# Performance work log

Measured on AMD Instinct MI355X. Metric: run time of the kernel, lower is better.

The kernel has to match this reference:

```python
import jax, jax.numpy as jnp
import numpy as np

B, S, D = 2, 2048, 1024
H, HD = 16, 64          # num_heads, head_dim = D // H
C = 8                   # subspace_dim of the equivariant relative-position basis
EPS = 1e-6              # flax LayerNorm default epsilon


def setup_inputs() -> dict:
    key = jax.random.key(0)
    ks = jax.random.split(key, 12)
    sd = 0.02
    return {
        "x": jax.random.normal(ks[0], (B, S, D), jnp.float32),
        "Q_basis": jax.random.normal(ks[1], (S, S, C), jnp.float32),
        "Wq": jax.random.normal(ks[2], (D, H, HD), jnp.float32) * sd,
        "bq": jnp.zeros((H, HD), jnp.float32),
        "Wk": jax.random.normal(ks[3], (D, H, HD), jnp.float32) * sd,
        "bk": jnp.zeros((H, HD), jnp.float32),
        "Wv": jax.random.normal(ks[4], (D, H, HD), jnp.float32) * sd,
        "bv": jnp.zeros((H, HD), jnp.float32),
        "q_ln_scale": jnp.ones((HD,), jnp.float32),
        "k_ln_scale": jnp.ones((HD,), jnp.float32),
        "relative_attn": jax.random.normal(ks[5], (C, H), jnp.float32) * sd,
        "Wo": jax.random.normal(ks[6], (H, HD, D), jnp.float32) * sd,
        "bo": jnp.zeros((D,), jnp.float32),
    }


def _layernorm(x, scale):
    # LayerNorm over last axis, use_bias=False
    mu = jnp.mean(x, axis=-1, keepdims=True)
    var = jnp.mean(jnp.square(x - mu), axis=-1, keepdims=True)
    return (x - mu) * jax.lax.rsqrt(var + EPS) * scale


def reference(x, Q_basis, Wq, bq, Wk, bk, Wv, bv,
              q_ln_scale, k_ln_scale, relative_attn, Wo, bo):
    # QKV projections: [B,S,D] x [D,H,HD] -> [B,S,H,HD]
    q = jnp.einsum('bsd,dhk->bshk', x, Wq) + bq
    k = jnp.einsum('bsd,dhk->bshk', x, Wk) + bk
    v = jnp.einsum('bsd,dhk->bshk', x, Wv) + bv
    # QK layernorm over head_dim
    q = _layernorm(q, q_ln_scale)
    k = _layernorm(k, k_ln_scale)
    # Learned relative-position bias: [C,H] x [S,S,C] -> [H,S,S]
    bias = jnp.einsum('ch,qkc->hqk', relative_attn, Q_basis)
    # Scaled dot-product attention with bias (matches nn.dot_product_attention)
    scores = jnp.einsum('bqhd,bkhd->bhqk', q, k) / jnp.sqrt(jnp.float32(HD))
    attn = jax.nn.softmax(scores + bias, axis=-1)
    ctx = jnp.einsum('bhqk,bkhd->bqhd', attn, v)
    # Output projection over (heads, head_dim) -> D
    return jnp.einsum('bqhd,hdo->bqo', ctx, Wo) + bo
```

## Files before the change

kernel.cpp:

```cpp
#include <hip/hip_runtime.h>

typedef float f32x4 __attribute__((ext_vector_type(4)));
typedef __bf16 bf16x8 __attribute__((ext_vector_type(8)));
typedef unsigned short u16x8 __attribute__((ext_vector_type(8)));
typedef unsigned short u16x4 __attribute__((ext_vector_type(4)));

#define AS1 __attribute__((address_space(1)))
#define AS3 __attribute__((address_space(3)))

static __device__ __forceinline__ void gll16(const void* g, void* l) {
  __builtin_amdgcn_global_load_lds((const AS1 void*)g, (AS3 void*)l, 16, 0, 0);
}

static __device__ __forceinline__ float bf2f(unsigned short u) {
  unsigned int x = ((unsigned int)u) << 16;
  float f; __builtin_memcpy(&f, &x, 4); return f;
}
static __device__ __forceinline__ unsigned short f2bf(float f) {
  unsigned int x; __builtin_memcpy(&x, &f, 4);
  unsigned int r = (x + 0x7fffu + ((x >> 16) & 1u)) >> 16;
  return (unsigned short)r;
}

#define LOG2E 1.4426950408889634f
#define QSCALE (0.125f * LOG2E)

__global__ __launch_bounds__(256) void k_cvt_x(const float* __restrict__ x,
                                               unsigned short* __restrict__ xb) {
  int i = (blockIdx.x * 256 + threadIdx.x) * 4;
  float4 v = *(const float4*)(x + i);
  u16x4 o; o.x = f2bf(v.x); o.y = f2bf(v.y); o.z = f2bf(v.z); o.w = f2bf(v.w);
  *(u16x4*)(xb + i) = o;
}

__global__ __launch_bounds__(256) void k_transpose(const float* __restrict__ w0,
                                                   const float* __restrict__ w1,
                                                   const float* __restrict__ w2,
                                                   const float* __restrict__ w3,
                                                   unsigned short* __restrict__ dqkv,
                                                   unsigned short* __restrict__ dwo) {
  __shared__ float tile[32][33];
  int z = blockIdx.z;
  const float* src = (z == 0) ? w0 : (z == 1) ? w1 : (z == 2) ? w2 : w3;
  unsigned short* dst = (z < 3) ? (dqkv + (size_t)z * 1024 * 1024) : dwo;
  int tx = threadIdx.x, ty = threadIdx.y;
  int x0 = blockIdx.x * 32, y0 = blockIdx.y * 32;
#pragma unroll
  for (int i = 0; i < 4; ++i)
    tile[ty + 8 * i][tx] = src[(size_t)(y0 + ty + 8 * i) * 1024 + x0 + tx];
  __syncthreads();
#pragma unroll
  for (int i = 0; i < 4; ++i)
    dst[(size_t)(x0 + ty + 8 * i) * 1024 + y0 + tx] = f2bf(tile[tx][ty + 8 * i]);
}

__global__ __launch_bounds__(256) void k_bias(const float* __restrict__ Qb,
                                              const float* __restrict__ R,
                                              unsigned short* __restrict__ bias) {
  __shared__ float Rs[8][16];
  int t = threadIdx.x;
  if (t < 128) Rs[t >> 4][t & 15] = R[t] * LOG2E;
  __syncthreads();
  int q = blockIdx.x;
  int k = t * 8;
  const float* src = Qb + ((size_t)q * 2048 + k) * 8;
  float a[8][8];
#pragma unroll
  for (int kk = 0; kk < 8; ++kk) {
    float4 lo = *(const float4*)(src + kk * 8);
    float4 hi = *(const float4*)(src + kk * 8 + 4);
    a[kk][0] = lo.x; a[kk][1] = lo.y; a[kk][2] = lo.z; a[kk][3] = lo.w;
    a[kk][4] = hi.x; a[kk][5] = hi.y; a[kk][6] = hi.z; a[kk][7] = hi.w;
  }
#pragma unroll
  for (int h = 0; h < 16; ++h) {
    u16x8 o;
#pragma unroll
    for (int kk = 0; kk < 8; ++kk) {
      float s = 0.f;
#pragma unroll
      for (int c = 0; c < 8; ++c) s += a[kk][c] * Rs[c][h];
      o[kk] = f2bf(s);
    }
    *(u16x8*)(bias + ((size_t)h * 2048 + q) * 2048 + k) = o;
  }
}

__global__ __launch_bounds__(256) void k_qkv(const unsigned short* __restrict__ xb,
                                             const unsigned short* __restrict__ wt,
                                             const float* __restrict__ bq,
                                             const float* __restrict__ bk,
                                             const float* __restrict__ bv,
                                             const float* __restrict__ qls,
                                             const float* __restrict__ kls,
                                             unsigned short* __restrict__ qo,
                                             unsigned short* __restrict__ kqo,
                                             unsigned short* __restrict__ vo) {
  __shared__ __align__(16) unsigned short As[8192];
  __shared__ __align__(16) unsigned short Bs[8192];
  const int tid = threadIdx.x;
  const int w = tid >> 6, lane = tid & 63, quad = lane >> 4, lx = lane & 15;
  const int m0 = blockIdx.y * 128, n0 = blockIdx.x * 128;
  const int wrow = w >> 1, wcol = w & 1;

  f32x4 acc[4][4];
#pragma unroll
  for (int i = 0; i < 4; ++i)
#pragma unroll
    for (int j = 0; j < 4; ++j) acc[i][j] = (f32x4){0.f, 0.f, 0.f, 0.f};

  const unsigned short* ga = xb + (size_t)(m0 + 32 * w + (lane >> 2)) * 1024 + (lane & 3) * 8;
  const unsigned short* gb = wt + (size_t)(n0 + 32 * w + (lane >> 2)) * 1024 + (lane & 3) * 8;

  gll16(ga, As + w * 1024);
  gll16(ga + 16 * 1024, As + w * 1024 + 512);
  gll16(gb, Bs + w * 1024);
  gll16(gb + 16 * 1024, Bs + w * 1024 + 512);
  __syncthreads();

  for (int kt = 0; kt < 32; ++kt) {
    const int cur = kt & 1;
    if (kt < 31) {
      const int kofs = (kt + 1) * 32;
      unsigned short* lan = As + (cur ^ 1) * 4096 + w * 1024;
      unsigned short* lbn = Bs + (cur ^ 1) * 4096 + w * 1024;
      gll16(ga + kofs, lan);
      gll16(ga + kofs + 16 * 1024, lan + 512);
      gll16(gb + kofs, lbn);
      gll16(gb + kofs + 16 * 1024, lbn + 512);
    }
    const unsigned short* ac = As + cur * 4096;
    const unsigned short* bc = Bs + cur * 4096;
    bf16x8 af[4], bfr[4];
#pragma unroll
    for (int i = 0; i < 4; ++i)
      af[i] = *(const bf16x8*)&ac[(64 * wrow + 16 * i + lx) * 32 + quad * 8];
#pragma unroll
    for (int j = 0; j < 4; ++j)
      bfr[j] = *(const bf16x8*)&bc[(64 * wcol + 16 * j + lx) * 32 + quad * 8];
    __builtin_amdgcn_s_setprio(1);
#pragma unroll
    for (int i = 0; i < 4; ++i)
#pragma unroll
      for (int j = 0; j < 4; ++j)
        acc[i][j] = __builtin_amdgcn_mfma_f32_16x16x32_bf16(af[i], bfr[j], acc[i][j], 0, 0, 0);
    __builtin_amdgcn_s_setprio(0);
    __syncthreads();
  }

  const int colbase = n0 + 64 * wcol;
  const int region = colbase >> 10;
  const int h = (colbase & 1023) >> 6;
  const float* pbp = (region == 0) ? bq : (region == 1) ? bk : bv;
  float pb[4];
#pragma unroll
  for (int j = 0; j < 4; ++j) pb[j] = pbp[h * 64 + j * 16 + lx];

  if (region == 2) {
#pragma unroll
    for (int i = 0; i < 4; ++i) {
#pragma unroll
      for (int rr = 0; rr < 4; ++rr) {
        int m = m0 + 64 * wrow + 16 * i + quad * 4 + rr;
        int b = m >> 11, s = m & 2047;
        unsigned short* dst = vo + ((size_t)b * 16 + h) * 64 * 2048 + s;
#pragma unroll
        for (int j = 0; j < 4; ++j)
          dst[(size_t)(j * 16 + lx) * 2048] = f2bf(acc[i][j][rr] + pb[j]);
      }
    }
  } else {
    const float fac = region ? 1.0f : QSCALE;
    float scl[4];
    const float* lsp = region ? kls : qls;
#pragma unroll
    for (int j = 0; j < 4; ++j) scl[j] = lsp[j * 16 + lx] * fac;
    unsigned short* base = region ? kqo : qo;
#pragma unroll
    for (int i = 0; i < 4; ++i) {
#pragma unroll
      for (int rr = 0; rr < 4; ++rr) {
        int m = m0 + 64 * wrow + 16 * i + quad * 4 + rr;
        int b = m >> 11, s = m & 2047;
        float v0 = acc[i][0][rr] + pb[0];
        float v1 = acc[i][1][rr] + pb[1];
        float v2 = acc[i][2][rr] + pb[2];
        float v3 = acc[i][3][rr] + pb[3];
        float s1 = v0 + v1 + v2 + v3;
        float s2 = v0 * v0 + v1 * v1 + v2 * v2 + v3 * v3;
#pragma unroll
        for (int d = 1; d < 16; d <<= 1) {
          s1 += __shfl_xor(s1, d, 64);
          s2 += __shfl_xor(s2, d, 64);
        }
        float mu = s1 * 0.015625f;
        float var = s2 * 0.015625f - mu * mu;
        float ri = __builtin_amdgcn_rsqf(var + 1e-6f);
        unsigned short* dst = base + (((size_t)b * 16 + h) * 2048 + s) * 64;
        dst[0 * 16 + lx] = f2bf((v0 - mu) * ri * scl[0]);
        dst[1 * 16 + lx] = f2bf((v1 - mu) * ri * scl[1]);
        dst[2 * 16 + lx] = f2bf((v2 - mu) * ri * scl[2]);
        dst[3 * 16 + lx] = f2bf((v3 - mu) * ri * scl[3]);
      }
    }
  }
}

__global__ __launch_bounds__(256) void k_attn(const unsigned short* __restrict__ qp,
                                              const unsigned short* __restrict__ kp,
                                              const unsigned short* __restrict__ vp,
                                              const unsigned short* __restrict__ bp,
                                              unsigned short* __restrict__ ctx) {
  __shared__ __align__(16) unsigned short QPs[4096];
  __shared__ __align__(16) unsigned short Ks[8192];
  __shared__ __align__(16) unsigned short Vs[8192];
  const int tid = threadIdx.x;
  const int w = tid >> 6, lane = tid & 63, quad = lane >> 4, lx = lane & 15;
  const int lx7 = lane & 7;
  const int qt = blockIdx.x, h = blockIdx.y, b = blockIdx.z;
  const int q0 = qt * 64;
  const size_t bh = (size_t)b * 16 + h;

  const unsigned short* qg = qp + (bh * 2048 + q0) * 64;
  gll16(qg + w * 512 + lane * 8, QPs + w * 512);
  gll16(qg + 2048 + w * 512 + lane * 8, QPs + 2048 + w * 512);

  const unsigned short* kg = kp + bh * 2048 * 64;
  const unsigned short* vg = vp + bh * 64 * 2048;
  const unsigned short* bg = bp + ((size_t)h * 2048 + q0 + 16 * w + quad * 4) * 2048 + lx;

  const int rA = 16 * w + (lane >> 3);
  const int cA = (lane & 7) ^ (rA & 7);
  const unsigned short* kgA = kg + (size_t)rA * 64 + cA * 8;
  const unsigned short* kgB = kg + (size_t)(rA + 8) * 64 + cA * 8;
  const unsigned short* vgA = vg + (size_t)rA * 2048 + cA * 8;
  const unsigned short* vgB = vg + (size_t)(rA + 8) * 2048 + cA * 8;

  gll16(kgA, Ks + w * 1024);
  gll16(kgB, Ks + w * 1024 + 512);
  gll16(vgA, Vs + w * 1024);
  gll16(vgB, Vs + w * 1024 + 512);
  unsigned short bu[4][4], bun[4][4];
#pragma unroll
  for (int rr = 0; rr < 4; ++rr)
#pragma unroll
    for (int j = 0; j < 4; ++j) bu[rr][j] = bg[(size_t)rr * 2048 + j * 16];

  __syncthreads();

  bf16x8 qf[2];
#pragma unroll
  for (int hh = 0; hh < 2; ++hh)
    qf[hh] = *(const bf16x8*)&QPs[(16 * w + lx) * 64 + hh * 32 + quad * 8];

  float l_run[4] = {0.f, 0.f, 0.f, 0.f};
  f32x4 acco[4];
#pragma unroll
  for (int j = 0; j < 4; ++j) acco[j] = (f32x4){0.f, 0.f, 0.f, 0.f};

  for (int kt = 0; kt < 32; ++kt) {
    const int cur = kt & 1;
    const unsigned short* kc = Ks + cur * 4096;
    const unsigned short* vc = Vs + cur * 4096;
    if (kt < 31) {
      const size_t k1 = (size_t)(kt + 1) * 64;
      unsigned short* kn = Ks + (cur ^ 1) * 4096 + w * 1024;
      unsigned short* vn = Vs + (cur ^ 1) * 4096 + w * 1024;
      gll16(kgA + k1 * 64, kn);
      gll16(kgB + k1 * 64, kn + 512);
      gll16(vgA + k1, vn);
      gll16(vgB + k1, vn + 512);
#pragma unroll
      for (int rr = 0; rr < 4; ++rr)
#pragma unroll
        for (int j = 0; j < 4; ++j) bun[rr][j] = bg[(size_t)rr * 2048 + k1 + j * 16];
    }

    f32x4 accs[4];
#pragma unroll
    for (int j = 0; j < 4; ++j)
#pragma unroll
      for (int rr = 0; rr < 4; ++rr) accs[j][rr] = bf2f(bu[rr][j]);
    __builtin_amdgcn_s_setprio(1);
#pragma unroll
    for (int j = 0; j < 4; ++j) {
#pragma unroll
      for (int hh = 0; hh < 2; ++hh) {
        bf16x8 kf = *(const bf16x8*)&kc[(j * 16 + lx) * 64 + ((hh * 4 + quad) ^ lx7) * 8];
        accs[j] = __builtin_amdgcn_mfma_f32_16x16x32_bf16(qf[hh], kf, accs[j], 0, 0, 0);
      }
    }
    __builtin_amdgcn_s_setprio(0);

#pragma unroll
    for (int rr = 0; rr < 4; ++rr) {
      float p0 = __builtin_amdgcn_exp2f(accs[0][rr]);
      float p1 = __builtin_amdgcn_exp2f(accs[1][rr]);
      float p2 = __builtin_amdgcn_exp2f(accs[2][rr]);
      float p3 = __builtin_amdgcn_exp2f(accs[3][rr]);
      l_run[rr] += (p0 + p1) + (p2 + p3);
      const int q = quad * 4 + rr;
      const int swz = q & 7;
      const int ch = lx >> 3;
      unsigned short* pw = QPs + w * 1024 + q * 64 + (lx & 7);
      pw[((ch ^ swz) << 3)]       = f2bf(p0);
      pw[(((ch + 2) ^ swz) << 3)] = f2bf(p1);
      pw[(((ch + 4) ^ swz) << 3)] = f2bf(p2);
      pw[(((ch + 6) ^ swz) << 3)] = f2bf(p3);
    }
    __asm__ volatile("s_waitcnt lgkmcnt(0)" ::: "memory");
    bf16x8 pf[2];
#pragma unroll
    for (int kh = 0; kh < 2; ++kh)
      pf[kh] = *(const bf16x8*)&QPs[w * 1024 + lx * 64 + (((kh * 4 + quad) ^ (lx & 7)) << 3)];
    __builtin_amdgcn_s_setprio(1);
#pragma unroll
    for (int j = 0; j < 4; ++j) {
#pragma unroll
      for (int kh = 0; kh < 2; ++kh) {
        bf16x8 vf = *(const bf16x8*)&vc[(j * 16 + lx) * 64 + ((kh * 4 + quad) ^ lx7) * 8];
        acco[j] = __builtin_amdgcn_mfma_f32_16x16x32_bf16(pf[kh], vf, acco[j], 0, 0, 0);
      }
    }
    __builtin_amdgcn_s_setprio(0);
    __syncthreads();
#pragma unroll
    for (int rr = 0; rr < 4; ++rr)
#pragma unroll
      for (int j = 0; j < 4; ++j) bu[rr][j] = bun[rr][j];
  }

#pragma unroll
  for (int rr = 0; rr < 4; ++rr) {
    float l = l_run[rr];
#pragma unroll
    for (int d = 1; d < 16; d <<= 1) l += __shfl_xor(l, d, 64);
    float rl = __builtin_amdgcn_rcpf(l);
    int s = q0 + 16 * w + quad * 4 + rr;
    unsigned short* dst = ctx + (((size_t)b * 2048 + s) * 16 + h) * 64;
#pragma unroll
    for (int j = 0; j < 4; ++j) dst[j * 16 + lx] = f2bf(acco[j][rr] * rl);
  }
}

__global__ __launch_bounds__(256) void k_out(const unsigned short* __restrict__ cx,
                                             const unsigned short* __restrict__ wt,
                                             const float* __restrict__ bo,
                                             float* __restrict__ out) {
  __shared__ __align__(16) unsigned short As[8192];
  __shared__ __align__(16) unsigned short Bs[8192];
  const int tid = threadIdx.x;
  const int w = tid >> 6, lane = tid & 63, quad = lane >> 4, lx = lane & 15;
  const int m0 = blockIdx.y * 128, n0 = blockIdx.x * 128;
  const int wrow = w >> 1, wcol = w & 1;

  f32x4 acc[4][4];
#pragma unroll
  for (int i = 0; i < 4; ++i)
#pragma unroll
    for (int j = 0; j < 4; ++j) acc[i][j] = (f32x4){0.f, 0.f, 0.f, 0.f};

  const unsigned short* ga = cx + (size_t)(m0 + 32 * w + (lane >> 2)) * 1024 + (lane & 3) * 8;
  const unsigned short* gb = wt + (size_t)(n0 + 32 * w + (lane >> 2)) * 1024 + (lane & 3) * 8;

  gll16(ga, As + w * 1024);
  gll16(ga + 16 * 1024, As + w * 1024 + 512);
  gll16(gb, Bs + w * 1024);
  gll16(gb + 16 * 1024, Bs + w * 1024 + 512);
  __syncthreads();

  for (int kt = 0; kt < 32; ++kt) {
    const int cur = kt & 1;
    if (kt < 31) {
      const int kofs = (kt + 1) * 32;
      unsigned short* lan = As + (cur ^ 1) * 4096 + w * 1024;
      unsigned short* lbn = Bs + (cur ^ 1) * 4096 + w * 1024;
      gll16(ga + kofs, lan);
      gll16(ga + kofs + 16 * 1024, lan + 512);
      gll16(gb + kofs, lbn);
      gll16(gb + kofs + 16 * 1024, lbn + 512);
    }
    const unsigned short* ac = As + cur * 4096;
    const unsigned short* bc = Bs + cur * 4096;
    bf16x8 af[4], bfr[4];
#pragma unroll
    for (int i = 0; i < 4; ++i)
      af[i] = *(const bf16x8*)&ac[(64 * wrow + 16 * i + lx) * 32 + quad * 8];
#pragma unroll
    for (int j = 0; j < 4; ++j)
      bfr[j] = *(const bf16x8*)&bc[(64 * wcol + 16 * j + lx) * 32 + quad * 8];
    __builtin_amdgcn_s_setprio(1);
#pragma unroll
    for (int i = 0; i < 4; ++i)
#pragma unroll
      for (int j = 0; j < 4; ++j)
        acc[i][j] = __builtin_amdgcn_mfma_f32_16x16x32_bf16(af[i], bfr[j], acc[i][j], 0, 0, 0);
    __builtin_amdgcn_s_setprio(0);
    __syncthreads();
  }

  const int colbase = n0 + 64 * wcol;
  float bb[4];
#pragma unroll
  for (int j = 0; j < 4; ++j) bb[j] = bo[colbase + j * 16 + lx];
#pragma unroll
  for (int i = 0; i < 4; ++i) {
#pragma unroll
    for (int rr = 0; rr < 4; ++rr) {
      int m = m0 + 64 * wrow + 16 * i + quad * 4 + rr;
      float* dst = out + (size_t)m * 1024 + colbase;
#pragma unroll
      for (int j = 0; j < 4; ++j) dst[j * 16 + lx] = acc[i][j][rr] + bb[j];
    }
  }
}

extern "C" void kernel_launch(void* const* d_in, const int* in_sizes, int n_in,
                              void* d_out, int out_size, void* d_ws, size_t ws_size,
                              hipStream_t stream) {
  (void)in_sizes; (void)n_in; (void)out_size; (void)ws_size;
  const float* x   = (const float*)d_in[0];
  const float* Qb  = (const float*)d_in[1];
  const float* Wq  = (const float*)d_in[2];
  const float* bq  = (const float*)d_in[3];
  const float* Wk  = (const float*)d_in[4];
  const float* bk  = (const float*)d_in[5];
  const float* Wv  = (const float*)d_in[6];
  const float* bv  = (const float*)d_in[7];
  const float* qls = (const float*)d_in[8];
  const float* kls = (const float*)d_in[9];
  const float* Ra  = (const float*)d_in[10];
  const float* Wo  = (const float*)d_in[11];
  const float* bo  = (const float*)d_in[12];
  float* out = (float*)d_out;

  char* ws = (char*)d_ws;
  unsigned short* xb    = (unsigned short*)(ws + 0);
  unsigned short* wqkvt = (unsigned short*)(ws + 8388608);
  unsigned short* wot   = (unsigned short*)(ws + 14680064);
  unsigned short* qb    = (unsigned short*)(ws + 16777216);
  unsigned short* kb    = (unsigned short*)(ws + 25165824);
  unsigned short* vtb   = (unsigned short*)(ws + 33554432);
  unsigned short* ctxb  = (unsigned short*)(ws + 41943040);
  unsigned short* biasb = (unsigned short*)(ws + 50331648);

  k_cvt_x<<<4096, 256, 0, stream>>>(x, xb);
  k_transpose<<<dim3(32, 32, 4), dim3(32, 8), 0, stream>>>(Wq, Wk, Wv, Wo, wqkvt, wot);
  k_bias<<<2048, 256, 0, stream>>>(Qb, Ra, biasb);
  k_qkv<<<dim3(24, 32), 256, 0, stream>>>(xb, wqkvt, bq, bk, bv, qls, kls, qb, kb, vtb);
  k_attn<<<dim3(32, 16, 2), 256, 0, stream>>>(qb, kb, vtb, biasb, ctxb);
  k_out<<<dim3(8, 32), 256, 0, stream>>>(ctxb, wot, bo, out);
}
```

Baseline: 436.0 us.

## Transpose score MFMA in attention for vector bias/P accesses; shrink out-proj N tile

The attention kernel swaps the MFMA operands so each lane holds four consecutive key columns for one query row. The bias can then be loaded as u16x4 vectors, P written to LDS as 8-byte stores, and the row-sum reduced with fewer shuffles. The output projection tile shrinks from 128x128 to 128x64, doubling the grid to 512 blocks for better CU occupancy at the cost of more A-tile reloads. f2bf is also switched to the native bf16 conversion.

```diff
diff --git a/kernel.cpp b/kernel.cpp
--- a/kernel.cpp
+++ b/kernel.cpp
@@ -17,9 +17,8 @@
   float f; __builtin_memcpy(&f, &x, 4); return f;
 }
 static __device__ __forceinline__ unsigned short f2bf(float f) {
-  unsigned int x; __builtin_memcpy(&x, &f, 4);
-  unsigned int r = (x + 0x7fffu + ((x >> 16) & 1u)) >> 16;
-  return (unsigned short)r;
+  __bf16 h = (__bf16)f;
+  unsigned short u; __builtin_memcpy(&u, &h, 2); return u;
 }
 
 #define LOG2E 1.4426950408889634f
@@ -227,7 +226,7 @@
 
   const unsigned short* kg = kp + bh * 2048 * 64;
   const unsigned short* vg = vp + bh * 64 * 2048;
-  const unsigned short* bg = bp + ((size_t)h * 2048 + q0 + 16 * w + quad * 4) * 2048 + lx;
+  const unsigned short* bg = bp + ((size_t)h * 2048 + q0 + 16 * w + lx) * 2048 + quad * 4;
 
   const int rA = 16 * w + (lane >> 3);
   const int cA = (lane & 7) ^ (rA & 7);
@@ -240,11 +239,9 @@
   gll16(kgB, Ks + w * 1024 + 512);
   gll16(vgA, Vs + w * 1024);
   gll16(vgB, Vs + w * 1024 + 512);
-  unsigned short bu[4][4], bun[4][4];
-#pragma unroll
-  for (int rr = 0; rr < 4; ++rr)
-#pragma unroll
-    for (int j = 0; j < 4; ++j) bu[rr][j] = bg[(size_t)rr * 2048 + j * 16];
+  u16x4 bu[4], bun[4];
+#pragma unroll
+  for (int j = 0; j < 4; ++j) bu[j] = *(const u16x4*)(bg + j * 16);
 
   __syncthreads();
 
@@ -253,7 +250,7 @@
   for (int hh = 0; hh < 2; ++hh)
     qf[hh] = *(const bf16x8*)&QPs[(16 * w + lx) * 64 + hh * 32 + quad * 8];
 
-  float l_run[4] = {0.f, 0.f, 0.f, 0.f};
+  float l_run = 0.f;
   f32x4 acco[4];
 #pragma unroll
   for (int j = 0; j < 4; ++j) acco[j] = (f32x4){0.f, 0.f, 0.f, 0.f};
@@ -271,48 +268,41 @@
       gll16(vgA + k1, vn);
       gll16(vgB + k1, vn + 512);
 #pragma unroll
-      for (int rr = 0; rr < 4; ++rr)
-#pragma unroll
-        for (int j = 0; j < 4; ++j) bun[rr][j] = bg[(size_t)rr * 2048 + k1 + j * 16];
+      for (int j = 0; j < 4; ++j) bun[j] = *(const u16x4*)(bg + k1 + j * 16);
     }
 
     f32x4 accs[4];
 #pragma unroll
     for (int j = 0; j < 4; ++j)
 #pragma unroll
-      for (int rr = 0; rr < 4; ++rr) accs[j][rr] = bf2f(bu[rr][j]);
+      for (int rr = 0; rr < 4; ++rr) accs[j][rr] = bf2f(bu[j][rr]);
     __builtin_amdgcn_s_setprio(1);
 #pragma unroll
     for (int j = 0; j < 4; ++j) {
 #pragma unroll
       for (int hh = 0; hh < 2; ++hh) {
         bf16x8 kf = *(const bf16x8*)&kc[(j * 16 + lx) * 64 + ((hh * 4 + quad) ^ lx7) * 8];
-        accs[j] = __builtin_amdgcn_mfma_f32_16x16x32_bf16(qf[hh], kf, accs[j], 0, 0, 0);
+        accs[j] = __builtin_amdgcn_mfma_f32_16x16x32_bf16(kf, qf[hh], accs[j], 0, 0, 0);
       }
     }
     __builtin_amdgcn_s_setprio(0);
 
 #pragma unroll
-    for (int rr = 0; rr < 4; ++rr) {
-      float p0 = __builtin_amdgcn_exp2f(accs[0][rr]);
-      float p1 = __builtin_amdgcn_exp2f(accs[1][rr]);
-      float p2 = __builtin_amdgcn_exp2f(accs[2][rr]);
-      float p3 = __builtin_amdgcn_exp2f(accs[3][rr]);
-      l_run[rr] += (p0 + p1) + (p2 + p3);
-      const int q = quad * 4 + rr;
-      const int swz = q & 7;
-      const int ch = lx >> 3;
-      unsigned short* pw = QPs + w * 1024 + q * 64 + (lx & 7);
-      pw[((ch ^ swz) << 3)]       = f2bf(p0);
-      pw[(((ch + 2) ^ swz) << 3)] = f2bf(p1);
-      pw[(((ch + 4) ^ swz) << 3)] = f2bf(p2);
-      pw[(((ch + 6) ^ swz) << 3)] = f2bf(p3);
+    for (int j = 0; j < 4; ++j) {
+      float p0 = __builtin_amdgcn_exp2f(accs[j][0]);
+      float p1 = __builtin_amdgcn_exp2f(accs[j][1]);
+      float p2 = __builtin_amdgcn_exp2f(accs[j][2]);
+      float p3 = __builtin_amdgcn_exp2f(accs[j][3]);
+      l_run += (p0 + p1) + (p2 + p3);
+      u16x4 pv; pv.x = f2bf(p0); pv.y = f2bf(p1); pv.z = f2bf(p2); pv.w = f2bf(p3);
+      const int pc = (2 * j + (quad >> 1)) ^ lx7;
+      *(u16x4*)&QPs[w * 1024 + lx * 64 + pc * 8 + (quad & 1) * 4] = pv;
     }
     __asm__ volatile("s_waitcnt lgkmcnt(0)" ::: "memory");
     bf16x8 pf[2];
 #pragma unroll
     for (int kh = 0; kh < 2; ++kh)
-      pf[kh] = *(const bf16x8*)&QPs[w * 1024 + lx * 64 + (((kh * 4 + quad) ^ (lx & 7)) << 3)];
+      pf[kh] = *(const bf16x8*)&QPs[w * 1024 + lx * 64 + (((kh * 4 + quad) ^ lx7) << 3)];
     __builtin_amdgcn_s_setprio(1);
 #pragma unroll
     for (int j = 0; j < 4; ++j) {
@@ -325,16 +315,14 @@
     __builtin_amdgcn_s_setprio(0);
     __syncthreads();
 #pragma unroll
-    for (int rr = 0; rr < 4; ++rr)
-#pragma unroll
-      for (int j = 0; j < 4; ++j) bu[rr][j] = bun[rr][j];
-  }
-
+    for (int j = 0; j < 4; ++j) bu[j] = bun[j];
+  }
+
+  l_run += __shfl_xor(l_run, 16, 64);
+  l_run += __shfl_xor(l_run, 32, 64);
 #pragma unroll
   for (int rr = 0; rr < 4; ++rr) {
-    float l = l_run[rr];
-#pragma unroll
-    for (int d = 1; d < 16; d <<= 1) l += __shfl_xor(l, d, 64);
+    float l = __shfl(l_run, quad * 4 + rr, 64);
     float rl = __builtin_amdgcn_rcpf(l);
     int s = q0 + 16 * w + quad * 4 + rr;
     unsigned short* dst = ctx + (((size_t)b * 2048 + s) * 16 + h) * 64;
@@ -348,25 +336,24 @@
                                              const float* __restrict__ bo,
                                              float* __restrict__ out) {
   __shared__ __align__(16) unsigned short As[8192];
-  __shared__ __align__(16) unsigned short Bs[8192];
+  __shared__ __align__(16) unsigned short Bs[4096];
   const int tid = threadIdx.x;
   const int w = tid >> 6, lane = tid & 63, quad = lane >> 4, lx = lane & 15;
-  const int m0 = blockIdx.y * 128, n0 = blockIdx.x * 128;
+  const int m0 = blockIdx.y * 128, n0 = blockIdx.x * 64;
   const int wrow = w >> 1, wcol = w & 1;
 
-  f32x4 acc[4][4];
+  f32x4 acc[4][2];
 #pragma unroll
   for (int i = 0; i < 4; ++i)
 #pragma unroll
-    for (int j = 0; j < 4; ++j) acc[i][j] = (f32x4){0.f, 0.f, 0.f, 0.f};
+    for (int j = 0; j < 2; ++j) acc[i][j] = (f32x4){0.f, 0.f, 0.f, 0.f};
 
   const unsigned short* ga = cx + (size_t)(m0 + 32 * w + (lane >> 2)) * 1024 + (lane & 3) * 8;
-  const unsigned short* gb = wt + (size_t)(n0 + 32 * w + (lane >> 2)) * 1024 + (lane & 3) * 8;
+  const unsigned short* gb = wt + (size_t)(n0 + 16 * w + (lane >> 2)) * 1024 + (lane & 3) * 8;
 
   gll16(ga, As + w * 1024);
   gll16(ga + 16 * 1024, As + w * 1024 + 512);
-  gll16(gb, Bs + w * 1024);
-  gll16(gb + 16 * 1024, Bs + w * 1024 + 512);
+  gll16(gb, Bs + w * 512);
   __syncthreads();
 
   for (int kt = 0; kt < 32; ++kt) {
@@ -374,35 +361,33 @@
     if (kt < 31) {
       const int kofs = (kt + 1) * 32;
       unsigned short* lan = As + (cur ^ 1) * 4096 + w * 1024;
-      unsigned short* lbn = Bs + (cur ^ 1) * 4096 + w * 1024;
       gll16(ga + kofs, lan);
       gll16(ga + kofs + 16 * 1024, lan + 512);
-      gll16(gb + kofs, lbn);
-      gll16(gb + kofs + 16 * 1024, lbn + 512);
+      gll16(gb + kofs, Bs + (cur ^ 1) * 2048 + w * 512);
     }
     const unsigned short* ac = As + cur * 4096;
-    const unsigned short* bc = Bs + cur * 4096;
-    bf16x8 af[4], bfr[4];
+    const unsigned short* bc = Bs + cur * 2048;
+    bf16x8 af[4], bfr[2];
 #pragma unroll
     for (int i = 0; i < 4; ++i)
       af[i] = *(const bf16x8*)&ac[(64 * wrow + 16 * i + lx) * 32 + quad * 8];
 #pragma unroll
-    for (int j = 0; j < 4; ++j)
-      bfr[j] = *(const bf16x8*)&bc[(64 * wcol + 16 * j + lx) * 32 + quad * 8];
+    for (int j = 0; j < 2; ++j)
+      bfr[j] = *(const bf16x8*)&bc[(32 * wcol + 16 * j + lx) * 32 + quad * 8];
     __builtin_amdgcn_s_setprio(1);
 #pragma unroll
     for (int i = 0; i < 4; ++i)
 #pragma unroll
-      for (int j = 0; j < 4; ++j)
+      for (int j = 0; j < 2; ++j)
         acc[i][j] = __builtin_amdgcn_mfma_f32_16x16x32_bf16(af[i], bfr[j], acc[i][j], 0, 0, 0);
     __builtin_amdgcn_s_setprio(0);
     __syncthreads();
   }
 
-  const int colbase = n0 + 64 * wcol;
-  float bb[4];
-#pragma unroll
-  for (int j = 0; j < 4; ++j) bb[j] = bo[colbase + j * 16 + lx];
+  const int colbase = n0 + 32 * wcol;
+  float bb[2];
+#pragma unroll
+  for (int j = 0; j < 2; ++j) bb[j] = bo[colbase + j * 16 + lx];
 #pragma unroll
   for (int i = 0; i < 4; ++i) {
 #pragma unroll
@@ -410,7 +395,7 @@
       int m = m0 + 64 * wrow + 16 * i + quad * 4 + rr;
       float* dst = out + (size_t)m * 1024 + colbase;
 #pragma unroll
-      for (int j = 0; j < 4; ++j) dst[j * 16 + lx] = acc[i][j][rr] + bb[j];
+      for (int j = 0; j < 2; ++j) dst[j * 16 + lx] = acc[i][j][rr] + bb[j];
     }
   }
 }
@@ -449,5 +434,5 @@
   k_bias<<<2048, 256, 0, stream>>>(Qb, Ra, biasb);
   k_qkv<<<dim3(24, 32), 256, 0, stream>>>(xb, wqkvt, bq, bk, bv, qls, kls, qb, kb, vtb);
   k_attn<<<dim3(32, 16, 2), 256, 0, stream>>>(qb, kb, vtb, biasb, ctxb);
-  k_out<<<dim3(8, 32), 256, 0, stream>>>(ctxb, wot, bo, out);
-}
+  k_out<<<dim3(16, 32), 256, 0, stream>>>(ctxb, wot, bo, out);
+}
```

After: 453.3 us. +4.0%, slower.
